# Kernel optimization log

Hardware: AMD Instinct MI355X
Metric: run time of the kernel (lower is better)

The kernel has to match this reference:

```python
import jax, jax.numpy as jnp
import numpy as np

NUM_HEADS = 8
NUM_KV_HEADS = 1
HEAD_DIM = 256
HIDDEN = 2048
LAYER_INDEX = 5
SOFTCAP = 50.0
SCALING = HEAD_DIM ** -0.5
MAX_SEQ = 8192
NUM_LAYERS = 26
POS = 4096
NEG_INF = -1e9


def rotate_half(x):
    x1, x2 = jnp.split(x, 2, axis=-1)
    return jnp.concatenate((-x2, x1), axis=-1)


def ane_rmsnorm(x, w):
    # ANE-friendly RMSNorm: scale by per-row max before squaring, unit offset weight
    maxval = jnp.clip(jnp.max(jnp.abs(x), axis=-1, keepdims=True), 2.0 ** -24, None)
    xs = x / maxval
    rs = jax.lax.rsqrt(jnp.sum(xs * xs, axis=-1, keepdims=True))
    return rs * (x.shape[-1] ** 0.5) * xs * (1.0 + w)


def setup_inputs() -> dict:
    key = jax.random.key(0)
    ks = jax.random.split(key, 7)
    hidden_states = jax.random.normal(ks[0], (1, HIDDEN, 1, 1), jnp.float32)
    qkv_w = jax.random.normal(ks[1], ((NUM_HEADS + 2 * NUM_KV_HEADS) * HEAD_DIM, HIDDEN), jnp.float32) * 0.02
    o_w = jax.random.normal(ks[2], (HIDDEN, NUM_HEADS * HEAD_DIM), jnp.float32) * 0.02
    q_norm_w = jax.random.normal(ks[3], (HEAD_DIM,), jnp.float32) * 0.1
    k_norm_w = jax.random.normal(ks[4], (HEAD_DIM,), jnp.float32) * 0.1
    k_cache = jax.random.normal(ks[5], (NUM_LAYERS, NUM_KV_HEADS, MAX_SEQ, HEAD_DIM), jnp.float32)
    v_cache = jax.random.normal(ks[6], (NUM_LAYERS, NUM_KV_HEADS, MAX_SEQ, HEAD_DIM), jnp.float32)
    half = HEAD_DIM // 2
    inv_freq = 1.0 / (10000.0 ** (jnp.arange(half, dtype=jnp.float32) / half))
    freqs = POS * inv_freq
    emb = jnp.concatenate((freqs, freqs))
    cos = jnp.cos(emb).reshape(1, 1, 1, HEAD_DIM)
    sin = jnp.sin(emb).reshape(1, 1, 1, HEAD_DIM)
    valid = jnp.arange(MAX_SEQ) <= POS
    mask = jnp.where(valid, 0.0, NEG_INF).astype(jnp.float32).reshape(1, 1, 1, MAX_SEQ)
    return dict(hidden_states=hidden_states, cos=cos, sin=sin, kv_write_indices=POS,
                k_cache=k_cache, v_cache=v_cache, mask=mask,
                qkv_w=qkv_w, o_w=o_w, q_norm_w=q_norm_w, k_norm_w=k_norm_w)


def reference(hidden_states, cos, sin, kv_write_indices, k_cache, v_cache, mask,
              qkv_w, o_w, q_norm_w, k_norm_w):
    B = hidden_states.shape[0]
    L = hidden_states.shape[-1]  # 1 (single-token decode)
    # 1x1 conv == linear over channel dim
    qkv = jnp.einsum('oc,bchl->bohl', qkv_w, hidden_states)
    qkv = qkv.reshape(B, NUM_HEADS + 2 * NUM_KV_HEADS, HEAD_DIM, L).transpose(0, 1, 3, 2)  # (B,H,L,D)
    xq = qkv[:, :NUM_HEADS]
    xk = qkv[:, NUM_HEADS:NUM_HEADS + NUM_KV_HEADS]
    xv = qkv[:, NUM_HEADS + NUM_KV_HEADS:]
    xk = ane_rmsnorm(xk, k_norm_w)
    xk = xk * cos + rotate_half(xk) * sin
    xq = ane_rmsnorm(xq, q_norm_w)
    xq = (xq * cos + rotate_half(xq) * sin) * SCALING
    # KV-cache write at current position
    k_cache = jax.lax.dynamic_update_slice(k_cache, xk, (LAYER_INDEX, 0, kv_write_indices, 0))
    v_cache = jax.lax.dynamic_update_slice(v_cache, xv, (LAYER_INDEX, 0, kv_write_indices, 0))
    keys = k_cache[LAYER_INDEX, 0]   # (S, D) single KV head (MQA)
    vals = v_cache[LAYER_INDEX, 0]   # (S, D)
    # all query heads attend to the shared KV head (vectorized over heads)
    scores = jnp.einsum('sd,bhqd->bhqs', keys, xq)
    scores = jnp.tanh(scores / SOFTCAP) * SOFTCAP
    scores = scores + mask  # (1,1,1,S) broadcast
    probs = jax.nn.softmax(scores, axis=-1)
    out = jnp.einsum('bhqs,sd->bhqd', probs, vals)  # (B,H,L,D)
    # head-major concat -> (B, H*D, 1, L), matching per-head permute(0,3,1,2)+cat
    out = out.transpose(0, 1, 3, 2).reshape(B, NUM_HEADS * HEAD_DIM, 1, L)
    return jnp.einsum('oc,bchl->bohl', o_w, out)
```

## Files before the change

kernel.cpp:

```cpp
#include <hip/hip_runtime.h>
#include <hip/hip_cooperative_groups.h>

namespace cg = cooperative_groups;

#define NUMH 8
#define HD 256
#define HID 2048
#define LIDX 5
#define MAXS 8192
#define NB 256
#define NT 256

__device__ __forceinline__ float wsum(float v) {
#pragma unroll
  for (int m = 32; m >= 1; m >>= 1) v += __shfl_xor(v, m, 64);
  return v;
}
__device__ __forceinline__ float wmax(float v) {
#pragma unroll
  for (int m = 32; m >= 1; m >>= 1) v = fmaxf(v, __shfl_xor(v, m, 64));
  return v;
}

__global__ __launch_bounds__(NT) void attn_fused(
    const float* __restrict__ hidden, const float* __restrict__ cosb,
    const float* __restrict__ sinb, const int* __restrict__ idxp,
    const float* __restrict__ kcache, const float* __restrict__ vcache,
    const float* __restrict__ qkvw, const float* __restrict__ ow,
    const float* __restrict__ qnw, const float* __restrict__ knw,
    float* __restrict__ out, float* __restrict__ ws) {
  cg::grid_group grid = cg::this_grid();
  const int tid = threadIdx.x;
  const int lane = tid & 63;
  const int wave = tid >> 6;
  const int blk = blockIdx.x;
  const int gw = blk * 4 + wave;

  float* ws_qkv = ws;
  float* ws_acc = ws + 2560;
  float* ws_l   = ws + 2560 + 2048;

  __shared__ float qs[NUMH][HD];
  __shared__ float ksh[HD];
  __shared__ float accsh[4][2048];
  __shared__ float lsh[4][8];

  if (blk == 0) {
    for (int i = tid; i < 2056; i += NT) ws_acc[i] = 0.0f;
  }

  float4 h4[8];
#pragma unroll
  for (int i = 0; i < 8; ++i) h4[i] = ((const float4*)hidden)[lane + 64 * i];
  for (int r = gw; r < 2560; r += NB * 4) {
    const float4* wr = (const float4*)(qkvw + (size_t)r * HID);
    float a = 0.f;
#pragma unroll
    for (int i = 0; i < 8; ++i) {
      float4 w4 = wr[lane + 64 * i];
      a += w4.x * h4[i].x + w4.y * h4[i].y + w4.z * h4[i].z + w4.w * h4[i].w;
    }
    a = wsum(a);
    if (lane == 0) ws_qkv[r] = a;
  }
  grid.sync();

  const int idx = idxp[0];
  for (int task = wave; task < 9; task += 4) {
    const bool isk = (task == 8);
    const float* src = ws_qkv + task * HD;
    const float* nw = isk ? knw : qnw;
    float4 x = ((const float4*)src)[lane];
    float m = fmaxf(fmaxf(fabsf(x.x), fabsf(x.y)), fmaxf(fabsf(x.z), fabsf(x.w)));
    m = wmax(m);
    m = fmaxf(m, 5.9604644775390625e-8f);
    float xs0 = x.x / m, xs1 = x.y / m, xs2 = x.z / m, xs3 = x.w / m;
    float ss = wsum(xs0 * xs0 + xs1 * xs1 + xs2 * xs2 + xs3 * xs3);
    float rs = rsqrtf(ss) * 16.0f;
    float4 nwv = ((const float4*)nw)[lane];
    float n0 = rs * xs0 * (1.f + nwv.x);
    float n1 = rs * xs1 * (1.f + nwv.y);
    float n2 = rs * xs2 * (1.f + nwv.z);
    float n3 = rs * xs3 * (1.f + nwv.w);
    float p0 = __shfl_xor(n0, 32, 64);
    float p1 = __shfl_xor(n1, 32, 64);
    float p2 = __shfl_xor(n2, 32, 64);
    float p3 = __shfl_xor(n3, 32, 64);
    float sgn = (lane < 32) ? -1.f : 1.f;
    float4 c4 = ((const float4*)cosb)[lane];
    float4 s4 = ((const float4*)sinb)[lane];
    float scl = isk ? 1.0f : 0.0625f;
    float4 o4;
    o4.x = (n0 * c4.x + sgn * p0 * s4.x) * scl;
    o4.y = (n1 * c4.y + sgn * p1 * s4.y) * scl;
    o4.z = (n2 * c4.z + sgn * p2 * s4.z) * scl;
    o4.w = (n3 * c4.w + sgn * p3 * s4.w) * scl;
    float* dst = isk ? ksh : qs[task];
    ((float4*)dst)[lane] = o4;
  }
  __syncthreads();

  float4 qf[NUMH];
#pragma unroll
  for (int h = 0; h < NUMH; ++h) qf[h] = ((const float4*)qs[h])[lane];

  const int S = idx + 1;
  const int chunk = (S + NB - 1) / NB;
  const int s0 = blk * chunk;
  const int s1 = min(S, s0 + chunk);
  float4 av[NUMH];
  float lacc[NUMH];
#pragma unroll
  for (int h = 0; h < NUMH; ++h) {
    av[h] = make_float4(0.f, 0.f, 0.f, 0.f);
    lacc[h] = 0.f;
  }

  const float* kbase = kcache + (size_t)LIDX * MAXS * HD;
  const float* vbase = vcache + (size_t)LIDX * MAXS * HD;
  for (int s = s0 + wave; s < s1; s += 4) {
    float4 k4, v4;
    if (s == idx) {
      k4 = ((const float4*)ksh)[lane];
      v4 = ((const float4*)(ws_qkv + (NUMH + 1) * HD))[lane];
    } else {
      k4 = ((const float4*)(kbase + (size_t)s * HD))[lane];
      v4 = ((const float4*)(vbase + (size_t)s * HD))[lane];
    }
    float sc[NUMH];
#pragma unroll
    for (int h = 0; h < NUMH; ++h)
      sc[h] = qf[h].x * k4.x + qf[h].y * k4.y + qf[h].z * k4.z + qf[h].w * k4.w;
#pragma unroll
    for (int m = 32; m >= 1; m >>= 1) {
#pragma unroll
      for (int h = 0; h < NUMH; ++h) sc[h] += __shfl_xor(sc[h], m, 64);
    }
#pragma unroll
    for (int h = 0; h < NUMH; ++h) {
      float t = tanhf(sc[h] * 0.02f) * 50.0f;
      float p = __expf(t - 50.0f);
      lacc[h] += p;
      av[h].x += p * v4.x;
      av[h].y += p * v4.y;
      av[h].z += p * v4.z;
      av[h].w += p * v4.w;
    }
  }
#pragma unroll
  for (int h = 0; h < NUMH; ++h) ((float4*)&accsh[wave][h * HD])[lane] = av[h];
  if (lane == 0) {
#pragma unroll
    for (int h = 0; h < NUMH; ++h) lsh[wave][h] = lacc[h];
  }
  __syncthreads();
  for (int i = tid; i < 2048; i += NT) {
    float v = accsh[0][i] + accsh[1][i] + accsh[2][i] + accsh[3][i];
    atomicAdd(&ws_acc[i], v);
  }
  if (tid < 8) {
    float v = lsh[0][tid] + lsh[1][tid] + lsh[2][tid] + lsh[3][tid];
    atomicAdd(&ws_l[tid], v);
  }
  grid.sync();

  float* xsh = accsh[0];
  for (int i = tid; i < 2048; i += NT) xsh[i] = ws_acc[i] / ws_l[i >> 8];
  __syncthreads();
  for (int r = gw; r < 2048; r += NB * 4) {
    const float4* wr = (const float4*)(ow + (size_t)r * HID);
    float a = 0.f;
#pragma unroll
    for (int i = 0; i < 8; ++i) {
      float4 w4 = wr[lane + 64 * i];
      float4 x4 = ((const float4*)xsh)[lane + 64 * i];
      a += w4.x * x4.x + w4.y * x4.y + w4.z * x4.z + w4.w * x4.w;
    }
    a = wsum(a);
    if (lane == 0) out[r] = a;
  }
}

extern "C" void kernel_launch(void* const* d_in, const int* in_sizes, int n_in,
                              void* d_out, int out_size, void* d_ws, size_t ws_size,
                              hipStream_t stream) {
  const float* hidden = (const float*)d_in[0];
  const float* cosb   = (const float*)d_in[1];
  const float* sinb   = (const float*)d_in[2];
  const int*   idxp   = (const int*)d_in[3];
  const float* kcache = (const float*)d_in[4];
  const float* vcache = (const float*)d_in[5];
  const float* qkvw   = (const float*)d_in[7];
  const float* ow     = (const float*)d_in[8];
  const float* qnw    = (const float*)d_in[9];
  const float* knw    = (const float*)d_in[10];
  float* out = (float*)d_out;
  float* ws  = (float*)d_ws;

  void* args[] = {&hidden, &cosb, &sinb, &idxp, &kcache, &vcache,
                  &qkvw, &ow, &qnw, &knw, &out, &ws};
  hipLaunchCooperativeKernel(attn_fused, dim3(NB), dim3(NT), args, 0, stream);
}
```

Baseline: 459.4 us.

## Split cooperative fused kernel into three ordinary launches instead of grid syncs

```diff
diff --git a/kernel.cpp b/kernel.cpp
--- a/kernel.cpp
+++ b/kernel.cpp
@@ -1,15 +1,10 @@
 #include <hip/hip_runtime.h>
-#include <hip/hip_cooperative_groups.h>
-
-namespace cg = cooperative_groups;
 
 #define NUMH 8
 #define HD 256
 #define HID 2048
 #define LIDX 5
 #define MAXS 8192
-#define NB 256
-#define NT 256
 
 __device__ __forceinline__ float wsum(float v) {
 #pragma unroll
@@ -22,48 +17,51 @@
   return v;
 }
 
-__global__ __launch_bounds__(NT) void attn_fused(
-    const float* __restrict__ hidden, const float* __restrict__ cosb,
-    const float* __restrict__ sinb, const int* __restrict__ idxp,
-    const float* __restrict__ kcache, const float* __restrict__ vcache,
-    const float* __restrict__ qkvw, const float* __restrict__ ow,
-    const float* __restrict__ qnw, const float* __restrict__ knw,
-    float* __restrict__ out, float* __restrict__ ws) {
-  cg::grid_group grid = cg::this_grid();
+
+__global__ __launch_bounds__(256) void k_qkv(const float* __restrict__ qkvw,
+                                             const float* __restrict__ hidden,
+                                             float* __restrict__ ws) {
+  const int lane = threadIdx.x & 63;
+  const int wave = threadIdx.x >> 6;
+  if (blockIdx.x == 0) {
+    for (int i = threadIdx.x; i < 2056; i += 256) ws[2560 + i] = 0.0f;
+  }
+  const int r = blockIdx.x * 4 + wave;
+  const float4* wr = (const float4*)(qkvw + (size_t)r * HID);
+  const float4* h = (const float4*)hidden;
+  float a = 0.f;
+#pragma unroll
+  for (int i = 0; i < 8; ++i) {
+    float4 w4 = wr[lane + 64 * i];
+    float4 h4 = h[lane + 64 * i];
+    a += w4.x * h4.x + w4.y * h4.y + w4.z * h4.z + w4.w * h4.w;
+  }
+  a = wsum(a);
+  if (lane == 0) ws[r] = a;
+}
+
+__global__ __launch_bounds__(256) void k_attn(const float* __restrict__ cosb,
+                                              const float* __restrict__ sinb,
+                                              const int* __restrict__ idxp,
+                                              const float* __restrict__ kcache,
+                                              const float* __restrict__ vcache,
+                                              const float* __restrict__ qnw,
+                                              const float* __restrict__ knw,
+                                              float* __restrict__ ws) {
   const int tid = threadIdx.x;
   const int lane = tid & 63;
   const int wave = tid >> 6;
   const int blk = blockIdx.x;
-  const int gw = blk * 4 + wave;
+  const int NB = gridDim.x;
 
   float* ws_qkv = ws;
   float* ws_acc = ws + 2560;
-  float* ws_l   = ws + 2560 + 2048;
+  float* ws_l = ws + 2560 + 2048;
 
   __shared__ float qs[NUMH][HD];
   __shared__ float ksh[HD];
   __shared__ float accsh[4][2048];
   __shared__ float lsh[4][8];
-
-  if (blk == 0) {
-    for (int i = tid; i < 2056; i += NT) ws_acc[i] = 0.0f;
-  }
-
-  float4 h4[8];
-#pragma unroll
-  for (int i = 0; i < 8; ++i) h4[i] = ((const float4*)hidden)[lane + 64 * i];
-  for (int r = gw; r < 2560; r += NB * 4) {
-    const float4* wr = (const float4*)(qkvw + (size_t)r * HID);
-    float a = 0.f;
-#pragma unroll
-    for (int i = 0; i < 8; ++i) {
-      float4 w4 = wr[lane + 64 * i];
-      a += w4.x * h4[i].x + w4.y * h4[i].y + w4.z * h4[i].z + w4.w * h4[i].w;
-    }
-    a = wsum(a);
-    if (lane == 0) ws_qkv[r] = a;
-  }
-  grid.sync();
 
   const int idx = idxp[0];
   for (int task = wave; task < 9; task += 4) {
@@ -154,7 +152,7 @@
     for (int h = 0; h < NUMH; ++h) lsh[wave][h] = lacc[h];
   }
   __syncthreads();
-  for (int i = tid; i < 2048; i += NT) {
+  for (int i = tid; i < 2048; i += 256) {
     float v = accsh[0][i] + accsh[1][i] + accsh[2][i] + accsh[3][i];
     atomicAdd(&ws_acc[i], v);
   }
@@ -162,23 +160,29 @@
     float v = lsh[0][tid] + lsh[1][tid] + lsh[2][tid] + lsh[3][tid];
     atomicAdd(&ws_l[tid], v);
   }
-  grid.sync();
-
-  float* xsh = accsh[0];
-  for (int i = tid; i < 2048; i += NT) xsh[i] = ws_acc[i] / ws_l[i >> 8];
-  __syncthreads();
-  for (int r = gw; r < 2048; r += NB * 4) {
-    const float4* wr = (const float4*)(ow + (size_t)r * HID);
-    float a = 0.f;
-#pragma unroll
-    for (int i = 0; i < 8; ++i) {
-      float4 w4 = wr[lane + 64 * i];
-      float4 x4 = ((const float4*)xsh)[lane + 64 * i];
-      a += w4.x * x4.x + w4.y * x4.y + w4.z * x4.z + w4.w * x4.w;
-    }
-    a = wsum(a);
-    if (lane == 0) out[r] = a;
-  }
+}
+
+__global__ __launch_bounds__(256) void k_oproj(const float* __restrict__ ow,
+                                               float* __restrict__ ws,
+                                               float* __restrict__ out) {
+  const int lane = threadIdx.x & 63;
+  const int wave = threadIdx.x >> 6;
+  const int r = blockIdx.x * 4 + wave;
+  const float* ws_acc = ws + 2560;
+  const float* ws_l = ws + 2560 + 2048;
+  const float4* wr = (const float4*)(ow + (size_t)r * HID);
+  const float4* x = (const float4*)ws_acc;
+  float a = 0.f;
+#pragma unroll
+  for (int i = 0; i < 8; ++i) {
+    float rl = 1.0f / ws_l[i];
+    float4 w4 = wr[lane + 64 * i];
+    float4 x4 = x[lane + 64 * i];
+    a += w4.x * (x4.x * rl) + w4.y * (x4.y * rl) + w4.z * (x4.z * rl) +
+         w4.w * (x4.w * rl);
+  }
+  a = wsum(a);
+  if (lane == 0) out[r] = a;
 }
 
 extern "C" void kernel_launch(void* const* d_in, const int* in_sizes, int n_in,
@@ -197,7 +201,7 @@
   float* out = (float*)d_out;
   float* ws  = (float*)d_ws;
 
-  void* args[] = {&hidden, &cosb, &sinb, &idxp, &kcache, &vcache,
-                  &qkvw, &ow, &qnw, &knw, &out, &ws};
-  hipLaunchCooperativeKernel(attn_fused, dim3(NB), dim3(NT), args, 0, stream);
-}
+  k_qkv<<<640, 256, 0, stream>>>(qkvw, hidden, ws);
+  k_attn<<<256, 256, 0, stream>>>(cosb, sinb, idxp, kcache, vcache, qnw, knw, ws);
+  k_oproj<<<512, 256, 0, stream>>>(ow, ws, out);
+}
```

New measurement: 379.5 us. -17.4%, faster.
